# Kernel tuning notes

Hardware: AMD Instinct MI355X
Metric: run time of the kernel (lower is better)

Reference implementation:

```python
import jax, jax.numpy as jnp
import numpy as np

B, S, A, C, M, CE = 2, 8, 24000, 80, 20, 7
POS_TH, NEG_TH = 0.5, 0.4
V0, V1 = 0.1, 0.2              # SSD encode variances
SL1_BETA = 1.0 / 9.0
ALPHA, GAMMA = 0.25, 2.0
CB_BETA = 0.9999
EPS = 1e-7


def point_form(cf):
    # (cx,cy,w,h) -> (x1,y1,x2,y2)
    return jnp.concatenate([cf[..., :2] - cf[..., 2:] * 0.5, cf[..., :2] + cf[..., 2:] * 0.5], -1)


def jaccard(a, b):
    # a: [M,4], b: [A,4] point form -> IoU [M,A]
    lt = jnp.maximum(a[:, None, :2], b[None, :, :2])
    rb = jnp.minimum(a[:, None, 2:], b[None, :, 2:])
    wh = jnp.clip(rb - lt, 0.0)
    inter = wh[..., 0] * wh[..., 1]
    aa = (a[:, 2] - a[:, 0]) * (a[:, 3] - a[:, 1])
    ab = (b[:, 2] - b[:, 0]) * (b[:, 3] - b[:, 1])
    return inter / (aa[:, None] + ab[None, :] - inter + 1e-10)


def encode(matched, anchors_cf):
    # matched: [A,4] point form gt, anchors_cf: [A,4] center form
    g_cxcy = ((matched[:, :2] + matched[:, 2:]) * 0.5 - anchors_cf[:, :2]) / (V0 * anchors_cf[:, 2:])
    g_wh = jnp.log(jnp.clip(matched[:, 2:] - matched[:, :2], 1e-6) / anchors_cf[:, 2:]) / V1
    return jnp.concatenate([g_cxcy, g_wh], -1)


def bce(p, y):
    p = jnp.clip(p, EPS, 1.0 - EPS)
    return -(y * jnp.log(p) + (1.0 - y) * jnp.log1p(-p))


def match_one(gtb, gtl, count, anchors_pf, anchors_cf):
    # SSD-style match with ignore band: conf in {-1 ignore, 0 background, i+1 positive matched to gt i}
    valid = jnp.arange(M) < count
    iou = jnp.where(valid[:, None], jaccard(gtb, anchors_pf), -1.0)  # [M,A]
    best_prior_idx = jnp.argmax(iou, axis=1)                         # best anchor per gt
    best_truth_iou = jnp.max(iou, axis=0)                            # best gt per anchor
    best_truth_idx = jnp.argmax(iou, axis=0)
    sidx = jnp.where(valid, best_prior_idx, A)                       # out-of-range -> dropped
    best_truth_iou = best_truth_iou.at[sidx].set(2.0, mode='drop')   # force each gt's best anchor positive
    best_truth_idx = best_truth_idx.at[sidx].set(jnp.arange(M), mode='drop')
    conf = (best_truth_idx + 1).astype(jnp.int32)                    # dummy labels = gt index
    conf = jnp.where(best_truth_iou < POS_TH, -1, conf)
    conf = jnp.where(best_truth_iou < NEG_TH, 0, conf)
    loc = encode(gtb[best_truth_idx], anchors_cf)
    has = count > 0
    conf = jnp.where(has, conf, -1)                                  # empty frame -> all ignore
    loc = jnp.where(has, loc, 0.0)
    # gather per-anchor multi-hot labels: labels_bs = [zeros; gt_labels][dumy_conf]
    lab = jnp.where((conf > 0)[:, None], gtl[jnp.clip(conf - 1, 0, M - 1)], 0.0)
    return conf, loc, lab


def setup_inputs() -> dict:
    key = jax.random.key(0)
    ks = jax.random.split(key, 10)
    confidence = jax.random.normal(ks[0], (B, S, A, C), jnp.float32)
    predicted_locations = jax.random.normal(ks[1], (B, S, A, 4), jnp.float32)
    gc = jax.random.uniform(ks[2], (B, S, M, 2))
    gw = jax.random.uniform(ks[3], (B, S, M, 2), minval=0.05, maxval=0.4)
    gt_boxes = jnp.clip(jnp.concatenate([gc - gw * 0.5, gc + gw * 0.5], -1), 0.0, 1.0)
    gt_labels = (jax.random.uniform(ks[4], (B, S, M, C)) < 0.05).astype(jnp.float32)
    counts = jax.random.randint(ks[5], (B, S), 0, M + 1, jnp.int32)
    ac = jax.random.uniform(ks[6], (A, 2))
    aw = jax.random.uniform(ks[7], (A, 2), minval=0.02, maxval=0.3)
    anchors = jnp.concatenate([ac, aw], -1)  # center form (cx,cy,w,h)
    ego_preds = jax.random.normal(ks[8], (B, S, CE), jnp.float32)
    ego_labels = jax.random.randint(ks[9], (B, S), 0, CE, jnp.int32)
    cls_num_list = jax.random.randint(jax.random.fold_in(key, 11), (C,), 1, 10000, jnp.int32)
    return {"confidence": confidence, "predicted_locations": predicted_locations,
            "gt_boxes": gt_boxes, "gt_labels": gt_labels, "counts": counts,
            "anchors": anchors, "ego_preds": ego_preds, "ego_labels": ego_labels,
            "cls_num_list": cls_num_list}


def reference(confidence, predicted_locations, gt_boxes, gt_labels, counts, anchors, ego_preds, ego_labels, cls_num_list):
    preds = jax.nn.sigmoid(confidence)
    anchors_pf = point_form(anchors)
    flat = lambda x: x.reshape((B * S,) + x.shape[2:])
    conf_t, loc_t, lab_t = jax.vmap(match_one, in_axes=(0, 0, 0, None, None))(
        flat(gt_boxes), flat(gt_labels), counts.reshape(-1), anchors_pf, anchors)
    labels_bin = jax.lax.stop_gradient(conf_t.reshape(B, S, A).astype(jnp.float32))
    gt_locations = jax.lax.stop_gradient(loc_t.reshape(B, S, A, 4))
    all_labels = jax.lax.stop_gradient(lab_t.reshape(B, S, A, C))

    pos = (labels_bin > 0).astype(jnp.float32)
    num_pos = jnp.maximum(1.0, pos.sum())
    n = jnp.abs(predicted_locations - gt_locations)
    sl1 = jnp.where(n < SL1_BETA, 0.5 * n * n / SL1_BETA, n - 0.5 * SL1_BETA)
    regression_loss = (sl1 * pos[..., None]).sum() / (num_pos * 4.0)

    # class-balanced focal loss (module hardcodes gamma=1 inside sigmoid_cb_focal_loss)
    cmask = (labels_bin > -1).astype(jnp.float32)[..., None]
    w = (1.0 - CB_BETA) / (1.0 - jnp.power(jnp.float32(CB_BETA), cls_num_list.astype(jnp.float32)))
    w = w / w.sum()
    y = all_labels
    pt = preds * y + (1.0 - preds) * (1.0 - y)
    cb = w * y + (1.0 - CB_BETA) * (1.0 - y)
    cls_loss = (bce(preds, y) * cb * (1.0 - pt) * cmask).sum() / num_pos

    # ego focal loss (replicates original get_one_hot_labels column semantics)
    ep = jax.nn.sigmoid(ego_preds)
    evalid = ego_labels > -1
    col = (jnp.where(evalid[..., None], jax.nn.one_hot(ego_labels, CE), 0.0).sum((0, 1)) > 0).astype(jnp.float32)
    oh = jnp.broadcast_to(col, ep.shape)
    af = ALPHA * oh + (1.0 - ALPHA) * (1.0 - oh)
    ept = ep * oh + (1.0 - ep) * (1.0 - oh)
    n_ego = evalid.sum().astype(jnp.float32)
    ego_sum = (bce(ep, oh) * af * (1.0 - ept) ** GAMMA * evalid[..., None].astype(jnp.float32)).sum()
    ego_loss = jnp.where(n_ego > 0, ego_sum / jnp.maximum(n_ego, 1.0), 0.0)

    return regression_loss, cls_loss / 8.0 + ego_loss / 4.0
```

## Files before the change

kernel.cpp:

```cpp
#include <hip/hip_runtime.h>
#include <math.h>

#define NB 2
#define NS 8
#define NA 24000
#define NC 80
#define NM 20
#define NCE 7
#define NBS (NB*NS)
#define CPB 75
#define APC (NA/CPB)

#define POS_TH 0.5f
#define NEG_TH 0.4f
#define OMB 1e-4f
#define SL1B (1.0f/9.0f)

__device__ inline unsigned long long packKey(float f, unsigned idx) {
    unsigned u = __float_as_uint(f);
    u = (u & 0x80000000u) ? ~u : (u | 0x80000000u);
    return ((unsigned long long)u << 32) | (unsigned long long)(0xFFFFFFFFu - idx);
}

__global__ void __launch_bounds__(256)
k_mega(const float* __restrict__ gtb, const int* __restrict__ counts,
       const float* __restrict__ anchors, const float* __restrict__ ploc,
       const float* __restrict__ gtl, const float* __restrict__ logits,
       const int* __restrict__ cls_num, unsigned long long* __restrict__ gbest,
       double* __restrict__ acc, int* __restrict__ npos) {
    __shared__ float sg[NM][5];
    __shared__ unsigned long long sk[4][NM];
    __shared__ double sb[4];
    __shared__ float wsh[NC];
    __shared__ float wsum_sh;
    __shared__ unsigned qpos[APC];
    __shared__ unsigned qign[APC];
    __shared__ int npq, nqi;
    __shared__ float sf[4], sc[4];
    __shared__ int si[4];

    int bid = blockIdx.x;
    int role = bid % 3;
    int u = bid / 3;
    int bs = u / CPB, chunk = u % CPB;
    int t = threadIdx.x;
    int cnt = counts[bs];
    int a0 = chunk * APC;
    int wave = t >> 6, lane = t & 63;

    if (cnt == 0) return;

    if (role == 0) {
        const float4* x4p = (const float4*)logits + ((size_t)bs * NA + a0) * (NC / 4);
        double bg = 0.0;
        #pragma unroll
        for (int g = 0; g < 5; g++) {
            float4 xs[5];
            #pragma unroll
            for (int j = 0; j < 5; j++) xs[j] = x4p[t + (g * 5 + j) * 256];
            #pragma unroll
            for (int j = 0; j < 5; j++) {
                float xv[4] = {xs[j].x, xs[j].y, xs[j].z, xs[j].w};
                float tsum = 0.0f;
                #pragma unroll
                for (int jj = 0; jj < 4; jj++) {
                    float x = xv[jj];
                    float e = __expf(-x);
                    float s = 1.0f + e;
                    float pr = __builtin_amdgcn_rcpf(s);
                    float ls = __logf(s);
                    tsum += (x + ls) * pr;
                }
                bg += (double)tsum;
            }
        }
        #pragma unroll
        for (int off = 32; off > 0; off >>= 1) bg += __shfl_xor(bg, off);
        if (lane == 0) sb[wave] = bg;
        __syncthreads();
        if (t == 0) atomicAdd(&acc[1], (double)OMB * (sb[0] + sb[1] + sb[2] + sb[3]));
        return;
    }

    if (role == 2) {
        if (t < NM) {
            const float* g = gtb + ((size_t)bs * NM + t) * 4;
            float x1 = g[0], y1 = g[1], x2 = g[2], y2 = g[3];
            sg[t][0] = x1; sg[t][1] = y1; sg[t][2] = x2; sg[t][3] = y2;
            sg[t][4] = (x2 - x1) * (y2 - y1);
        }
        __syncthreads();
        bool has2 = t < (APC - 256);
        float4 c1 = ((const float4*)anchors)[a0 + t];
        float bx1 = c1.x - c1.z * 0.5f, by1 = c1.y - c1.w * 0.5f;
        float bx2 = c1.x + c1.z * 0.5f, by2 = c1.y + c1.w * 0.5f;
        float bar = (bx2 - bx1) * (by2 - by1);
        float cx1 = 0, cy1 = 0, cx2 = 0, cy2 = 0, car = 0;
        if (has2) {
            float4 c2 = ((const float4*)anchors)[a0 + 256 + t];
            cx1 = c2.x - c2.z * 0.5f; cy1 = c2.y - c2.w * 0.5f;
            cx2 = c2.x + c2.z * 0.5f; cy2 = c2.y + c2.w * 0.5f;
            car = (cx2 - cx1) * (cy2 - cy1);
        }
        for (int m = 0; m < cnt; m++) {
            float gx1 = sg[m][0], gy1 = sg[m][1], gx2 = sg[m][2], gy2 = sg[m][3], gar = sg[m][4];
            float ltx = fmaxf(gx1, bx1), lty = fmaxf(gy1, by1);
            float rbx = fminf(gx2, bx2), rby = fminf(gy2, by2);
            float wx = fmaxf(rbx - ltx, 0.0f), wy = fmaxf(rby - lty, 0.0f);
            float inter = wx * wy;
            float iou = inter / (gar + bar - inter + 1e-10f);
            unsigned long long k = packKey(iou, (unsigned)(a0 + t));
            if (has2) {
                float ltx2 = fmaxf(gx1, cx1), lty2 = fmaxf(gy1, cy1);
                float rbx2 = fminf(gx2, cx2), rby2 = fminf(gy2, cy2);
                float wx2 = fmaxf(rbx2 - ltx2, 0.0f), wy2 = fmaxf(rby2 - lty2, 0.0f);
                float inter2 = wx2 * wy2;
                float iou2 = inter2 / (gar + car - inter2 + 1e-10f);
                unsigned long long k2 = packKey(iou2, (unsigned)(a0 + 256 + t));
                if (k2 > k) k = k2;
            }
            #pragma unroll
            for (int off = 32; off > 0; off >>= 1) {
                unsigned long long o = __shfl_xor(k, off);
                if (o > k) k = o;
            }
            if (lane == 0) sk[wave][m] = k;
        }
        __syncthreads();
        if (t < cnt) {
            unsigned long long k = sk[0][t];
            if (sk[1][t] > k) k = sk[1][t];
            if (sk[2][t] > k) k = sk[2][t];
            if (sk[3][t] > k) k = sk[3][t];
            atomicMax(&gbest[bs * NM + t], k);
        }
        return;
    }

    if (t == 0) { npq = 0; nqi = 0; }
    if (t < NM) {
        const float* g = gtb + ((size_t)bs * NM + t) * 4;
        float x1 = g[0], y1 = g[1], x2 = g[2], y2 = g[3];
        sg[t][0] = x1; sg[t][1] = y1; sg[t][2] = x2; sg[t][3] = y2;
        sg[t][4] = (x2 - x1) * (y2 - y1);
    }
    if (t < NC) {
        float n = (float)cls_num[t];
        wsh[t] = OMB / (1.0f - powf(0.9999f, n));
    }
    __syncthreads();
    if (t == 0) {
        float s = 0.0f;
        for (int c = 0; c < NC; c++) s += wsh[c];
        wsum_sh = s;
    }
    __syncthreads();
    if (t < NC) wsh[t] = wsh[t] / wsum_sh;

    float regsum = 0.0f;
    int pcnt = 0;
    for (int al = t; al < APC; al += 256) {
        int a = a0 + al;
        float4 cf = ((const float4*)anchors)[a];
        float ax1 = cf.x - cf.z * 0.5f, ay1 = cf.y - cf.w * 0.5f;
        float ax2 = cf.x + cf.z * 0.5f, ay2 = cf.y + cf.w * 0.5f;
        float aarea = (ax2 - ax1) * (ay2 - ay1);
        float best = -1.0f; int bm = 0;
        for (int m = 0; m < cnt; m++) {
            float ltx = fmaxf(sg[m][0], ax1), lty = fmaxf(sg[m][1], ay1);
            float rbx = fminf(sg[m][2], ax2), rby = fminf(sg[m][3], ay2);
            float wx = fmaxf(rbx - ltx, 0.0f), wy = fmaxf(rby - lty, 0.0f);
            float inter = wx * wy;
            float iou = inter / (sg[m][4] + aarea - inter + 1e-10f);
            if (iou > best) { best = iou; bm = m; }
        }
        int code = (best < NEG_TH) ? 0 : (best < POS_TH) ? -1 : bm + 1;
        if (code > 0) {
            pcnt++;
            size_t ia = (size_t)bs * NA + a;
            float mx1 = sg[bm][0], my1 = sg[bm][1], mx2 = sg[bm][2], my2 = sg[bm][3];
            float g0 = ((mx1 + mx2) * 0.5f - cf.x) / (0.1f * cf.z);
            float g1 = ((my1 + my2) * 0.5f - cf.y) / (0.1f * cf.w);
            float g2 = logf(fmaxf(mx2 - mx1, 1e-6f) / cf.z) / 0.2f;
            float g3 = logf(fmaxf(my2 - my1, 1e-6f) / cf.w) / 0.2f;
            float4 p = ((const float4*)ploc)[ia];
            float n0 = fabsf(p.x - g0), n1 = fabsf(p.y - g1);
            float n2 = fabsf(p.z - g2), n3 = fabsf(p.w - g3);
            float s0 = n0 < SL1B ? 0.5f * n0 * n0 / SL1B : n0 - 0.5f * SL1B;
            float s1 = n1 < SL1B ? 0.5f * n1 * n1 / SL1B : n1 - 0.5f * SL1B;
            float s2 = n2 < SL1B ? 0.5f * n2 * n2 / SL1B : n2 - 0.5f * SL1B;
            float s3 = n3 < SL1B ? 0.5f * n3 * n3 / SL1B : n3 - 0.5f * SL1B;
            regsum += s0 + s1 + s2 + s3;
            int q = atomicAdd(&npq, 1);
            qpos[q] = ((unsigned)bm << 16) | (unsigned)al;
        } else if (code == -1) {
            int q = atomicAdd(&nqi, 1);
            qign[q] = (unsigned)al;
        }
    }
    __syncthreads();

    float corrsum = 0.0f;
    int nq = npq, ni = nqi;
    for (int i = t; i < nq * 20; i += 256) {
        int qq = i / 20, c4 = i % 20;
        unsigned e = qpos[qq];
        int al = e & 0xFFFFu;
        int m  = (int)(e >> 16);
        float4 y4 = ((const float4*)(gtl + ((size_t)(bs * NM + m)) * NC))[c4];
        if (y4.x > 0.5f || y4.y > 0.5f || y4.z > 0.5f || y4.w > 0.5f) {
            float4 x4 = ((const float4*)logits)[((size_t)bs * NA + a0 + al) * (NC / 4) + c4];
            float yv[4] = {y4.x, y4.y, y4.z, y4.w};
            float xv[4] = {x4.x, x4.y, x4.z, x4.w};
            #pragma unroll
            for (int j = 0; j < 4; j++) {
                if (yv[j] > 0.5f) {
                    float x = xv[j];
                    float ee = __expf(-x);
                    float s = 1.0f + ee;
                    float pr = __builtin_amdgcn_rcpf(s);
                    float ls = __logf(s);
                    corrsum += ls * wsh[c4 * 4 + j] * (ee * pr)
                             - OMB * (x + ls) * pr;
                }
            }
        }
    }
    float negsum = 0.0f;
    for (int i = t; i < ni * 20; i += 256) {
        int qq = i / 20, c4 = i % 20;
        int al = (int)qign[qq];
        float4 x4 = ((const float4*)logits)[((size_t)bs * NA + a0 + al) * (NC / 4) + c4];
        float xv[4] = {x4.x, x4.y, x4.z, x4.w};
        float rs = 0.0f;
        #pragma unroll
        for (int j = 0; j < 4; j++) {
            float x = xv[j];
            float e = __expf(-x);
            float s = 1.0f + e;
            float pr = __builtin_amdgcn_rcpf(s);
            float ls = __logf(s);
            rs += (x + ls) * pr;
        }
        negsum += rs;
    }
    float clssum = corrsum - OMB * negsum;

    #pragma unroll
    for (int off = 32; off > 0; off >>= 1) {
        regsum += __shfl_xor(regsum, off);
        clssum += __shfl_xor(clssum, off);
        pcnt   += __shfl_xor(pcnt, off);
    }
    if (lane == 0) { sf[wave] = regsum; sc[wave] = clssum; si[wave] = pcnt; }
    __syncthreads();
    if (t == 0) {
        atomicAdd(&acc[0], (double)(sf[0] + sf[1] + sf[2] + sf[3]));
        atomicAdd(&acc[1], (double)(sc[0] + sc[1] + sc[2] + sc[3]));
        atomicAdd(npos, si[0] + si[1] + si[2] + si[3]);
    }
}

__global__ void __launch_bounds__(256)
k_final(const float* __restrict__ gtb, const int* __restrict__ counts,
        const float* __restrict__ anchors, const float* __restrict__ ploc,
        const float* __restrict__ gtl, const float* __restrict__ logits,
        const int* __restrict__ cls_num, const unsigned long long* __restrict__ gbest,
        const float* __restrict__ ego_preds, const int* __restrict__ ego_labels,
        const double* __restrict__ acc, const int* __restrict__ npos,
        float* __restrict__ out) {
    __shared__ float sg[NBS][NM][5];
    __shared__ unsigned sA[NBS][NM];
    __shared__ int scnt[NBS];
    __shared__ float wsh[NC];
    __shared__ float wsum_sh;
    __shared__ float scol[NCE];
    __shared__ float sdr[256], sdc[256];
    __shared__ int sdn[256];
    __shared__ float sred[256];
    __shared__ int sval[256];
    const float EPSF = 1e-7f;
    int t = threadIdx.x;

    if (t < NBS) scnt[t] = counts[t];
    if (t < NC) {
        float n = (float)cls_num[t];
        wsh[t] = OMB / (1.0f - powf(0.9999f, n));
    }
    if (t < NCE) {
        float c = 0.0f;
        for (int i = 0; i < NBS; i++) {
            int l = ego_labels[i];
            if (l > -1 && l == t) c = 1.0f;
        }
        scol[t] = c;
    }
    __syncthreads();
    if (t < NBS * NM) {
        int bs = t / NM, m = t % NM;
        const float* g = gtb + (size_t)t * 4;
        float x1 = g[0], y1 = g[1], x2 = g[2], y2 = g[3];
        sg[bs][m][0] = x1; sg[bs][m][1] = y1; sg[bs][m][2] = x2; sg[bs][m][3] = y2;
        sg[bs][m][4] = (x2 - x1) * (y2 - y1);
        sA[bs][m] = (m < scnt[bs])
            ? (unsigned)(0xFFFFFFFFu - (unsigned)(gbest[t] & 0xFFFFFFFFull))
            : 0xFFFFFFFFu;
    }
    if (t == 0) {
        float s = 0.0f;
        for (int c = 0; c < NC; c++) s += wsh[c];
        wsum_sh = s;
    }
    __syncthreads();
    if (t < NC) wsh[t] = wsh[t] / wsum_sh;
    __syncthreads();

    float dreg = 0.0f, dcls = 0.0f; int dnp = 0;
    if (t < NBS * NM) {
        int bs = t / NM, m = t % NM;
        int cnt = scnt[bs];
        if (m < cnt) {
            unsigned a = sA[bs][m];
            bool overridden = false;
            for (int m2 = m + 1; m2 < cnt; m2++)
                if (sA[bs][m2] == a) overridden = true;
            if (!overridden) {
                float4 cf = ((const float4*)anchors)[a];
                float ax1 = cf.x - cf.z * 0.5f, ay1 = cf.y - cf.w * 0.5f;
                float ax2 = cf.x + cf.z * 0.5f, ay2 = cf.y + cf.w * 0.5f;
                float aarea = (ax2 - ax1) * (ay2 - ay1);
                float best = -1.0f; int bm = 0;
                for (int m2 = 0; m2 < cnt; m2++) {
                    float ltx = fmaxf(sg[bs][m2][0], ax1), lty = fmaxf(sg[bs][m2][1], ay1);
                    float rbx = fminf(sg[bs][m2][2], ax2), rby = fminf(sg[bs][m2][3], ay2);
                    float wx = fmaxf(rbx - ltx, 0.0f), wy = fmaxf(rby - lty, 0.0f);
                    float inter = wx * wy;
                    float iou = inter / (sg[bs][m2][4] + aarea - inter + 1e-10f);
                    if (iou > best) { best = iou; bm = m2; }
                }
                int code = (best < NEG_TH) ? 0 : (best < POS_TH) ? -1 : bm + 1;
                if (!(code > 0 && bm == m)) {
                    size_t ia = (size_t)bs * NA + a;
                    float4 p = ((const float4*)ploc)[ia];
                    auto sl1 = [&](int mm) -> float {
                        float mx1 = sg[bs][mm][0], my1 = sg[bs][mm][1];
                        float mx2 = sg[bs][mm][2], my2 = sg[bs][mm][3];
                        float g0 = ((mx1 + mx2) * 0.5f - cf.x) / (0.1f * cf.z);
                        float g1 = ((my1 + my2) * 0.5f - cf.y) / (0.1f * cf.w);
                        float g2 = logf(fmaxf(mx2 - mx1, 1e-6f) / cf.z) / 0.2f;
                        float g3 = logf(fmaxf(my2 - my1, 1e-6f) / cf.w) / 0.2f;
                        float n0 = fabsf(p.x - g0), n1 = fabsf(p.y - g1);
                        float n2 = fabsf(p.z - g2), n3 = fabsf(p.w - g3);
                        float s0 = n0 < SL1B ? 0.5f * n0 * n0 / SL1B : n0 - 0.5f * SL1B;
                        float s1 = n1 < SL1B ? 0.5f * n1 * n1 / SL1B : n1 - 0.5f * SL1B;
                        float s2 = n2 < SL1B ? 0.5f * n2 * n2 / SL1B : n2 - 0.5f * SL1B;
                        float s3 = n3 < SL1B ? 0.5f * n3 * n3 / SL1B : n3 - 0.5f * SL1B;
                        return s0 + s1 + s2 + s3;
                    };
                    dreg += sl1(m);
                    if (code > 0) dreg -= sl1(bm);
                    else dnp += 1;
                    const float* xrow = logits + ia * NC;
                    const float* ynew = gtl + ((size_t)(bs * NM + m)) * NC;
                    const float* yold = gtl + ((size_t)(bs * NM + bm)) * NC;
                    bool addbg = (code == -1);
                    for (int c = 0; c < NC; c++) {
                        float x = xrow[c];
                        float e = __expf(-x);
                        float s = 1.0f + e;
                        float pr = __builtin_amdgcn_rcpf(s);
                        float ls = __logf(s);
                        float bgterm = OMB * (x + ls) * pr;
                        if (addbg) dcls += bgterm;
                        if (ynew[c] > 0.5f)
                            dcls += ls * wsh[c] * (e * pr) - bgterm;
                        if (code > 0 && yold[c] > 0.5f)
                            dcls -= ls * wsh[c] * (e * pr) - bgterm;
                    }
                }
            }
        }
    }
    sdr[t] = dreg; sdc[t] = dcls; sdn[t] = dnp;

    float term = 0.0f;
    if (t < NBS * NCE) {
        int bs = t / NCE, e = t % NCE;
        int lbl = ego_labels[bs];
        if (lbl > -1) {
            float x = ego_preds[t];
            float ep = 1.0f / (1.0f + expf(-x));
            float oh = scol[e];
            float af = 0.25f * oh + 0.75f * (1.0f - oh);
            float ept = ep * oh + (1.0f - ep) * (1.0f - oh);
            float epc = fminf(fmaxf(ep, EPSF), 1.0f - EPSF);
            float bce = -(oh * logf(epc) + (1.0f - oh) * log1pf(-epc));
            float om = 1.0f - ept;
            term = bce * af * om * om;
        }
    }
    sred[t] = term;
    sval[t] = (t < NBS && ego_labels[t] > -1) ? 1 : 0;
    __syncthreads();
    for (int off = 128; off > 0; off >>= 1) {
        if (t < off) {
            sdr[t] += sdr[t + off]; sdc[t] += sdc[t + off]; sdn[t] += sdn[t + off];
            sred[t] += sred[t + off]; sval[t] += sval[t + off];
        }
        __syncthreads();
    }
    if (t == 0) {
        float esum = sred[0];
        int ne = sval[0];
        float ego = (ne > 0) ? esum / (float)(ne > 1 ? ne : 1) : 0.0f;
        double npd = (double)(*npos + sdn[0]);
        if (npd < 1.0) npd = 1.0;
        double regT = acc[0] + (double)sdr[0];
        double clsT = acc[1] + (double)sdc[0];
        out[0] = (float)(regT / (npd * 4.0));
        out[1] = (float)(clsT / npd / 8.0 + (double)ego / 4.0);
    }
}

extern "C" void kernel_launch(void* const* d_in, const int* in_sizes, int n_in,
                              void* d_out, int out_size, void* d_ws, size_t ws_size,
                              hipStream_t stream) {
    const float* confidence = (const float*)d_in[0];
    const float* ploc       = (const float*)d_in[1];
    const float* gtb        = (const float*)d_in[2];
    const float* gtl        = (const float*)d_in[3];
    const int*   counts     = (const int*)d_in[4];
    const float* anchors    = (const float*)d_in[5];
    const float* ego_preds  = (const float*)d_in[6];
    const int*   ego_labels = (const int*)d_in[7];
    const int*   cls_num    = (const int*)d_in[8];
    float* out = (float*)d_out;

    char* ws = (char*)d_ws;
    double* acc  = (double*)ws;
    int* npos    = (int*)(ws + 16);
    unsigned long long* gbest = (unsigned long long*)(ws + 64);

    hipMemsetAsync(ws, 0, 4096, stream);
    k_mega<<<3 * NBS * CPB, 256, 0, stream>>>(gtb, counts, anchors, ploc, gtl,
                                              confidence, cls_num, gbest, acc, npos);
    k_final<<<1, 256, 0, stream>>>(gtb, counts, anchors, ploc, gtl, confidence,
                                   cls_num, gbest, ego_preds, ego_labels,
                                   acc, npos, out);
}
```

Baseline: 261.5 us.

## Replace global atomics and memset with per-block partials reduced in final kernel

Each block now writes its per-chunk best-anchor keys and its regression, classification and positive-count partials to dedicated workspace slots, instead of doing atomicAdd/atomicMax into shared global accumulators. The final single-block kernel reduces these partials, which removes the hipMemsetAsync launch and the global atomic contention. The background-logit loop is also restructured into a double-buffered issue/consume pattern to overlap loads with the transcendental math. In exchange, the final kernel must now scan 75 chunk entries per gt and about 3600 partials serially in one block.

New measurement: 244.6 us. 6.5% less time.

```diff
diff --git a/kernel.cpp b/kernel.cpp
--- a/kernel.cpp
+++ b/kernel.cpp
@@ -10,6 +10,7 @@
 #define NBS (NB*NS)
 #define CPB 75
 #define APC (NA/CPB)
+#define NUNITS (3*NBS*CPB)
 
 #define POS_TH 0.5f
 #define NEG_TH 0.4f
@@ -26,8 +27,9 @@
 k_mega(const float* __restrict__ gtb, const int* __restrict__ counts,
        const float* __restrict__ anchors, const float* __restrict__ ploc,
        const float* __restrict__ gtl, const float* __restrict__ logits,
-       const int* __restrict__ cls_num, unsigned long long* __restrict__ gbest,
-       double* __restrict__ acc, int* __restrict__ npos) {
+       const int* __restrict__ cls_num,
+       unsigned long long* __restrict__ chunkbest,
+       double* __restrict__ regp, double* __restrict__ clsp, int* __restrict__ npp) {
     __shared__ float sg[NM][5];
     __shared__ unsigned long long sk[4][NM];
     __shared__ double sb[4];
@@ -41,248 +43,262 @@
 
     int bid = blockIdx.x;
     int role = bid % 3;
-    int u = bid / 3;
-    int bs = u / CPB, chunk = u % CPB;
+    int unit = bid / 3;
+    int bs = unit / CPB, chunk = unit % CPB;
     int t = threadIdx.x;
     int cnt = counts[bs];
     int a0 = chunk * APC;
     int wave = t >> 6, lane = t & 63;
 
-    if (cnt == 0) return;
-
-    if (role == 0) {
-        const float4* x4p = (const float4*)logits + ((size_t)bs * NA + a0) * (NC / 4);
-        double bg = 0.0;
-        #pragma unroll
-        for (int g = 0; g < 5; g++) {
-            float4 xs[5];
+    double accReg = 0.0, accCls = 0.0;
+    int accNp = 0;
+
+    if (cnt != 0) {
+        if (role == 0) {
+            const float4* x4p = (const float4*)logits + ((size_t)bs * NA + a0) * (NC / 4);
+            float4 xa[5], xb[5];
+            double bg = 0.0;
+#define ISSUE(ARR,B) { _Pragma("unroll") \
+            for (int j = 0; j < 5; j++) ARR[j] = x4p[t + ((B)*5 + j)*256]; }
+#define CONSUME(ARR) { _Pragma("unroll") \
+            for (int j = 0; j < 5; j++) { \
+                float xv[4] = {ARR[j].x, ARR[j].y, ARR[j].z, ARR[j].w}; \
+                float tsum = 0.0f; \
+                _Pragma("unroll") \
+                for (int jj = 0; jj < 4; jj++) { \
+                    float x = xv[jj]; \
+                    float e = __expf(-x); \
+                    float s = 1.0f + e; \
+                    float pr = __builtin_amdgcn_rcpf(s); \
+                    float ls = __logf(s); \
+                    tsum += (x + ls) * pr; \
+                } \
+                bg += (double)tsum; \
+            } }
+            ISSUE(xa, 0);
+            ISSUE(xb, 1); CONSUME(xa);
+            ISSUE(xa, 2); CONSUME(xb);
+            ISSUE(xb, 3); CONSUME(xa);
+            ISSUE(xa, 4); CONSUME(xb);
+            CONSUME(xa);
+#undef ISSUE
+#undef CONSUME
             #pragma unroll
-            for (int j = 0; j < 5; j++) xs[j] = x4p[t + (g * 5 + j) * 256];
-            #pragma unroll
-            for (int j = 0; j < 5; j++) {
-                float xv[4] = {xs[j].x, xs[j].y, xs[j].z, xs[j].w};
-                float tsum = 0.0f;
+            for (int off = 32; off > 0; off >>= 1) bg += __shfl_xor(bg, off);
+            if (lane == 0) sb[wave] = bg;
+            __syncthreads();
+            if (t == 0) accCls = (double)OMB * (sb[0] + sb[1] + sb[2] + sb[3]);
+        } else if (role == 2) {
+            if (t < NM) {
+                const float* g = gtb + ((size_t)bs * NM + t) * 4;
+                float x1 = g[0], y1 = g[1], x2 = g[2], y2 = g[3];
+                sg[t][0] = x1; sg[t][1] = y1; sg[t][2] = x2; sg[t][3] = y2;
+                sg[t][4] = (x2 - x1) * (y2 - y1);
+            }
+            __syncthreads();
+            bool has2 = t < (APC - 256);
+            float4 c1 = ((const float4*)anchors)[a0 + t];
+            float bx1 = c1.x - c1.z * 0.5f, by1 = c1.y - c1.w * 0.5f;
+            float bx2 = c1.x + c1.z * 0.5f, by2 = c1.y + c1.w * 0.5f;
+            float bar = (bx2 - bx1) * (by2 - by1);
+            float cx1 = 0, cy1 = 0, cx2 = 0, cy2 = 0, car = 0;
+            if (has2) {
+                float4 c2 = ((const float4*)anchors)[a0 + 256 + t];
+                cx1 = c2.x - c2.z * 0.5f; cy1 = c2.y - c2.w * 0.5f;
+                cx2 = c2.x + c2.z * 0.5f; cy2 = c2.y + c2.w * 0.5f;
+                car = (cx2 - cx1) * (cy2 - cy1);
+            }
+            for (int m = 0; m < cnt; m++) {
+                float gx1 = sg[m][0], gy1 = sg[m][1], gx2 = sg[m][2], gy2 = sg[m][3], gar = sg[m][4];
+                float ltx = fmaxf(gx1, bx1), lty = fmaxf(gy1, by1);
+                float rbx = fminf(gx2, bx2), rby = fminf(gy2, by2);
+                float wx = fmaxf(rbx - ltx, 0.0f), wy = fmaxf(rby - lty, 0.0f);
+                float inter = wx * wy;
+                float iou = inter / (gar + bar - inter + 1e-10f);
+                unsigned long long k = packKey(iou, (unsigned)(a0 + t));
+                if (has2) {
+                    float ltx2 = fmaxf(gx1, cx1), lty2 = fmaxf(gy1, cy1);
+                    float rbx2 = fminf(gx2, cx2), rby2 = fminf(gy2, cy2);
+                    float wx2 = fmaxf(rbx2 - ltx2, 0.0f), wy2 = fmaxf(rby2 - lty2, 0.0f);
+                    float inter2 = wx2 * wy2;
+                    float iou2 = inter2 / (gar + car - inter2 + 1e-10f);
+                    unsigned long long k2 = packKey(iou2, (unsigned)(a0 + 256 + t));
+                    if (k2 > k) k = k2;
+                }
                 #pragma unroll
-                for (int jj = 0; jj < 4; jj++) {
-                    float x = xv[jj];
+                for (int off = 32; off > 0; off >>= 1) {
+                    unsigned long long o = __shfl_xor(k, off);
+                    if (o > k) k = o;
+                }
+                if (lane == 0) sk[wave][m] = k;
+            }
+            __syncthreads();
+            if (t < NM) {
+                unsigned long long k = 0ULL;
+                if (t < cnt) {
+                    k = sk[0][t];
+                    if (sk[1][t] > k) k = sk[1][t];
+                    if (sk[2][t] > k) k = sk[2][t];
+                    if (sk[3][t] > k) k = sk[3][t];
+                }
+                chunkbest[(size_t)unit * NM + t] = k;
+            }
+        } else {
+            if (t == 0) { npq = 0; nqi = 0; }
+            if (t < NM) {
+                const float* g = gtb + ((size_t)bs * NM + t) * 4;
+                float x1 = g[0], y1 = g[1], x2 = g[2], y2 = g[3];
+                sg[t][0] = x1; sg[t][1] = y1; sg[t][2] = x2; sg[t][3] = y2;
+                sg[t][4] = (x2 - x1) * (y2 - y1);
+            }
+            if (t < NC) {
+                float n = (float)cls_num[t];
+                wsh[t] = OMB / (1.0f - powf(0.9999f, n));
+            }
+            __syncthreads();
+            if (t == 0) {
+                float s = 0.0f;
+                for (int c = 0; c < NC; c++) s += wsh[c];
+                wsum_sh = s;
+            }
+            __syncthreads();
+            if (t < NC) wsh[t] = wsh[t] / wsum_sh;
+
+            float regsum = 0.0f;
+            int pcnt = 0;
+            for (int al = t; al < APC; al += 256) {
+                int a = a0 + al;
+                float4 cf = ((const float4*)anchors)[a];
+                float ax1 = cf.x - cf.z * 0.5f, ay1 = cf.y - cf.w * 0.5f;
+                float ax2 = cf.x + cf.z * 0.5f, ay2 = cf.y + cf.w * 0.5f;
+                float aarea = (ax2 - ax1) * (ay2 - ay1);
+                float best = -1.0f; int bm = 0;
+                for (int m = 0; m < cnt; m++) {
+                    float ltx = fmaxf(sg[m][0], ax1), lty = fmaxf(sg[m][1], ay1);
+                    float rbx = fminf(sg[m][2], ax2), rby = fminf(sg[m][3], ay2);
+                    float wx = fmaxf(rbx - ltx, 0.0f), wy = fmaxf(rby - lty, 0.0f);
+                    float inter = wx * wy;
+                    float iou = inter / (sg[m][4] + aarea - inter + 1e-10f);
+                    if (iou > best) { best = iou; bm = m; }
+                }
+                int code = (best < NEG_TH) ? 0 : (best < POS_TH) ? -1 : bm + 1;
+                if (code > 0) {
+                    pcnt++;
+                    size_t ia = (size_t)bs * NA + a;
+                    float mx1 = sg[bm][0], my1 = sg[bm][1], mx2 = sg[bm][2], my2 = sg[bm][3];
+                    float g0 = ((mx1 + mx2) * 0.5f - cf.x) / (0.1f * cf.z);
+                    float g1 = ((my1 + my2) * 0.5f - cf.y) / (0.1f * cf.w);
+                    float g2 = logf(fmaxf(mx2 - mx1, 1e-6f) / cf.z) / 0.2f;
+                    float g3 = logf(fmaxf(my2 - my1, 1e-6f) / cf.w) / 0.2f;
+                    float4 p = ((const float4*)ploc)[ia];
+                    float n0 = fabsf(p.x - g0), n1 = fabsf(p.y - g1);
+                    float n2 = fabsf(p.z - g2), n3 = fabsf(p.w - g3);
+                    float s0 = n0 < SL1B ? 0.5f * n0 * n0 / SL1B : n0 - 0.5f * SL1B;
+                    float s1 = n1 < SL1B ? 0.5f * n1 * n1 / SL1B : n1 - 0.5f * SL1B;
+                    float s2 = n2 < SL1B ? 0.5f * n2 * n2 / SL1B : n2 - 0.5f * SL1B;
+                    float s3 = n3 < SL1B ? 0.5f * n3 * n3 / SL1B : n3 - 0.5f * SL1B;
+                    regsum += s0 + s1 + s2 + s3;
+                    int q = atomicAdd(&npq, 1);
+                    qpos[q] = ((unsigned)bm << 16) | (unsigned)al;
+                } else if (code == -1) {
+                    int q = atomicAdd(&nqi, 1);
+                    qign[q] = (unsigned)al;
+                }
+            }
+            __syncthreads();
+
+            float corrsum = 0.0f;
+            int nq = npq, ni = nqi;
+            for (int i = t; i < nq * 20; i += 256) {
+                int qq = i / 20, c4 = i % 20;
+                unsigned e = qpos[qq];
+                int al = e & 0xFFFFu;
+                int m  = (int)(e >> 16);
+                float4 y4 = ((const float4*)(gtl + ((size_t)(bs * NM + m)) * NC))[c4];
+                if (y4.x > 0.5f || y4.y > 0.5f || y4.z > 0.5f || y4.w > 0.5f) {
+                    float4 x4 = ((const float4*)logits)[((size_t)bs * NA + a0 + al) * (NC / 4) + c4];
+                    float yv[4] = {y4.x, y4.y, y4.z, y4.w};
+                    float xv[4] = {x4.x, x4.y, x4.z, x4.w};
+                    #pragma unroll
+                    for (int j = 0; j < 4; j++) {
+                        if (yv[j] > 0.5f) {
+                            float x = xv[j];
+                            float ee = __expf(-x);
+                            float s = 1.0f + ee;
+                            float pr = __builtin_amdgcn_rcpf(s);
+                            float ls = __logf(s);
+                            corrsum += ls * wsh[c4 * 4 + j] * (ee * pr)
+                                     - OMB * (x + ls) * pr;
+                        }
+                    }
+                }
+            }
+            float negsum = 0.0f;
+            for (int i = t; i < ni * 20; i += 256) {
+                int qq = i / 20, c4 = i % 20;
+                int al = (int)qign[qq];
+                float4 x4 = ((const float4*)logits)[((size_t)bs * NA + a0 + al) * (NC / 4) + c4];
+                float xv[4] = {x4.x, x4.y, x4.z, x4.w};
+                float rs = 0.0f;
+                #pragma unroll
+                for (int j = 0; j < 4; j++) {
+                    float x = xv[j];
                     float e = __expf(-x);
                     float s = 1.0f + e;
                     float pr = __builtin_amdgcn_rcpf(s);
                     float ls = __logf(s);
-                    tsum += (x + ls) * pr;
-                }
-                bg += (double)tsum;
-            }
-        }
-        #pragma unroll
-        for (int off = 32; off > 0; off >>= 1) bg += __shfl_xor(bg, off);
-        if (lane == 0) sb[wave] = bg;
-        __syncthreads();
-        if (t == 0) atomicAdd(&acc[1], (double)OMB * (sb[0] + sb[1] + sb[2] + sb[3]));
-        return;
-    }
-
-    if (role == 2) {
-        if (t < NM) {
-            const float* g = gtb + ((size_t)bs * NM + t) * 4;
-            float x1 = g[0], y1 = g[1], x2 = g[2], y2 = g[3];
-            sg[t][0] = x1; sg[t][1] = y1; sg[t][2] = x2; sg[t][3] = y2;
-            sg[t][4] = (x2 - x1) * (y2 - y1);
-        }
-        __syncthreads();
-        bool has2 = t < (APC - 256);
-        float4 c1 = ((const float4*)anchors)[a0 + t];
-        float bx1 = c1.x - c1.z * 0.5f, by1 = c1.y - c1.w * 0.5f;
-        float bx2 = c1.x + c1.z * 0.5f, by2 = c1.y + c1.w * 0.5f;
-        float bar = (bx2 - bx1) * (by2 - by1);
-        float cx1 = 0, cy1 = 0, cx2 = 0, cy2 = 0, car = 0;
-        if (has2) {
-            float4 c2 = ((const float4*)anchors)[a0 + 256 + t];
-            cx1 = c2.x - c2.z * 0.5f; cy1 = c2.y - c2.w * 0.5f;
-            cx2 = c2.x + c2.z * 0.5f; cy2 = c2.y + c2.w * 0.5f;
-            car = (cx2 - cx1) * (cy2 - cy1);
-        }
-        for (int m = 0; m < cnt; m++) {
-            float gx1 = sg[m][0], gy1 = sg[m][1], gx2 = sg[m][2], gy2 = sg[m][3], gar = sg[m][4];
-            float ltx = fmaxf(gx1, bx1), lty = fmaxf(gy1, by1);
-            float rbx = fminf(gx2, bx2), rby = fminf(gy2, by2);
-            float wx = fmaxf(rbx - ltx, 0.0f), wy = fmaxf(rby - lty, 0.0f);
-            float inter = wx * wy;
-            float iou = inter / (gar + bar - inter + 1e-10f);
-            unsigned long long k = packKey(iou, (unsigned)(a0 + t));
-            if (has2) {
-                float ltx2 = fmaxf(gx1, cx1), lty2 = fmaxf(gy1, cy1);
-                float rbx2 = fminf(gx2, cx2), rby2 = fminf(gy2, cy2);
-                float wx2 = fmaxf(rbx2 - ltx2, 0.0f), wy2 = fmaxf(rby2 - lty2, 0.0f);
-                float inter2 = wx2 * wy2;
-                float iou2 = inter2 / (gar + car - inter2 + 1e-10f);
-                unsigned long long k2 = packKey(iou2, (unsigned)(a0 + 256 + t));
-                if (k2 > k) k = k2;
-            }
+                    rs += (x + ls) * pr;
+                }
+                negsum += rs;
+            }
+            float clssum = corrsum - OMB * negsum;
+
             #pragma unroll
             for (int off = 32; off > 0; off >>= 1) {
-                unsigned long long o = __shfl_xor(k, off);
-                if (o > k) k = o;
-            }
-            if (lane == 0) sk[wave][m] = k;
-        }
-        __syncthreads();
-        if (t < cnt) {
-            unsigned long long k = sk[0][t];
-            if (sk[1][t] > k) k = sk[1][t];
-            if (sk[2][t] > k) k = sk[2][t];
-            if (sk[3][t] > k) k = sk[3][t];
-            atomicMax(&gbest[bs * NM + t], k);
-        }
-        return;
-    }
-
-    if (t == 0) { npq = 0; nqi = 0; }
-    if (t < NM) {
-        const float* g = gtb + ((size_t)bs * NM + t) * 4;
-        float x1 = g[0], y1 = g[1], x2 = g[2], y2 = g[3];
-        sg[t][0] = x1; sg[t][1] = y1; sg[t][2] = x2; sg[t][3] = y2;
-        sg[t][4] = (x2 - x1) * (y2 - y1);
-    }
-    if (t < NC) {
-        float n = (float)cls_num[t];
-        wsh[t] = OMB / (1.0f - powf(0.9999f, n));
-    }
-    __syncthreads();
-    if (t == 0) {
-        float s = 0.0f;
-        for (int c = 0; c < NC; c++) s += wsh[c];
-        wsum_sh = s;
-    }
-    __syncthreads();
-    if (t < NC) wsh[t] = wsh[t] / wsum_sh;
-
-    float regsum = 0.0f;
-    int pcnt = 0;
-    for (int al = t; al < APC; al += 256) {
-        int a = a0 + al;
-        float4 cf = ((const float4*)anchors)[a];
-        float ax1 = cf.x - cf.z * 0.5f, ay1 = cf.y - cf.w * 0.5f;
-        float ax2 = cf.x + cf.z * 0.5f, ay2 = cf.y + cf.w * 0.5f;
-        float aarea = (ax2 - ax1) * (ay2 - ay1);
-        float best = -1.0f; int bm = 0;
-        for (int m = 0; m < cnt; m++) {
-            float ltx = fmaxf(sg[m][0], ax1), lty = fmaxf(sg[m][1], ay1);
-            float rbx = fminf(sg[m][2], ax2), rby = fminf(sg[m][3], ay2);
-            float wx = fmaxf(rbx - ltx, 0.0f), wy = fmaxf(rby - lty, 0.0f);
-            float inter = wx * wy;
-            float iou = inter / (sg[m][4] + aarea - inter + 1e-10f);
-            if (iou > best) { best = iou; bm = m; }
-        }
-        int code = (best < NEG_TH) ? 0 : (best < POS_TH) ? -1 : bm + 1;
-        if (code > 0) {
-            pcnt++;
-            size_t ia = (size_t)bs * NA + a;
-            float mx1 = sg[bm][0], my1 = sg[bm][1], mx2 = sg[bm][2], my2 = sg[bm][3];
-            float g0 = ((mx1 + mx2) * 0.5f - cf.x) / (0.1f * cf.z);
-            float g1 = ((my1 + my2) * 0.5f - cf.y) / (0.1f * cf.w);
-            float g2 = logf(fmaxf(mx2 - mx1, 1e-6f) / cf.z) / 0.2f;
-            float g3 = logf(fmaxf(my2 - my1, 1e-6f) / cf.w) / 0.2f;
-            float4 p = ((const float4*)ploc)[ia];
-            float n0 = fabsf(p.x - g0), n1 = fabsf(p.y - g1);
-            float n2 = fabsf(p.z - g2), n3 = fabsf(p.w - g3);
-            float s0 = n0 < SL1B ? 0.5f * n0 * n0 / SL1B : n0 - 0.5f * SL1B;
-            float s1 = n1 < SL1B ? 0.5f * n1 * n1 / SL1B : n1 - 0.5f * SL1B;
-            float s2 = n2 < SL1B ? 0.5f * n2 * n2 / SL1B : n2 - 0.5f * SL1B;
-            float s3 = n3 < SL1B ? 0.5f * n3 * n3 / SL1B : n3 - 0.5f * SL1B;
-            regsum += s0 + s1 + s2 + s3;
-            int q = atomicAdd(&npq, 1);
-            qpos[q] = ((unsigned)bm << 16) | (unsigned)al;
-        } else if (code == -1) {
-            int q = atomicAdd(&nqi, 1);
-            qign[q] = (unsigned)al;
-        }
-    }
-    __syncthreads();
-
-    float corrsum = 0.0f;
-    int nq = npq, ni = nqi;
-    for (int i = t; i < nq * 20; i += 256) {
-        int qq = i / 20, c4 = i % 20;
-        unsigned e = qpos[qq];
-        int al = e & 0xFFFFu;
-        int m  = (int)(e >> 16);
-        float4 y4 = ((const float4*)(gtl + ((size_t)(bs * NM + m)) * NC))[c4];
-        if (y4.x > 0.5f || y4.y > 0.5f || y4.z > 0.5f || y4.w > 0.5f) {
-            float4 x4 = ((const float4*)logits)[((size_t)bs * NA + a0 + al) * (NC / 4) + c4];
-            float yv[4] = {y4.x, y4.y, y4.z, y4.w};
-            float xv[4] = {x4.x, x4.y, x4.z, x4.w};
-            #pragma unroll
-            for (int j = 0; j < 4; j++) {
-                if (yv[j] > 0.5f) {
-                    float x = xv[j];
-                    float ee = __expf(-x);
-                    float s = 1.0f + ee;
-                    float pr = __builtin_amdgcn_rcpf(s);
-                    float ls = __logf(s);
-                    corrsum += ls * wsh[c4 * 4 + j] * (ee * pr)
-                             - OMB * (x + ls) * pr;
-                }
-            }
-        }
-    }
-    float negsum = 0.0f;
-    for (int i = t; i < ni * 20; i += 256) {
-        int qq = i / 20, c4 = i % 20;
-        int al = (int)qign[qq];
-        float4 x4 = ((const float4*)logits)[((size_t)bs * NA + a0 + al) * (NC / 4) + c4];
-        float xv[4] = {x4.x, x4.y, x4.z, x4.w};
-        float rs = 0.0f;
-        #pragma unroll
-        for (int j = 0; j < 4; j++) {
-            float x = xv[j];
-            float e = __expf(-x);
-            float s = 1.0f + e;
-            float pr = __builtin_amdgcn_rcpf(s);
-            float ls = __logf(s);
-            rs += (x + ls) * pr;
-        }
-        negsum += rs;
-    }
-    float clssum = corrsum - OMB * negsum;
-
-    #pragma unroll
-    for (int off = 32; off > 0; off >>= 1) {
-        regsum += __shfl_xor(regsum, off);
-        clssum += __shfl_xor(clssum, off);
-        pcnt   += __shfl_xor(pcnt, off);
-    }
-    if (lane == 0) { sf[wave] = regsum; sc[wave] = clssum; si[wave] = pcnt; }
-    __syncthreads();
-    if (t == 0) {
-        atomicAdd(&acc[0], (double)(sf[0] + sf[1] + sf[2] + sf[3]));
-        atomicAdd(&acc[1], (double)(sc[0] + sc[1] + sc[2] + sc[3]));
-        atomicAdd(npos, si[0] + si[1] + si[2] + si[3]);
-    }
+                regsum += __shfl_xor(regsum, off);
+                clssum += __shfl_xor(clssum, off);
+                pcnt   += __shfl_xor(pcnt, off);
+            }
+            if (lane == 0) { sf[wave] = regsum; sc[wave] = clssum; si[wave] = pcnt; }
+            __syncthreads();
+            if (t == 0) {
+                accReg = (double)(sf[0] + sf[1] + sf[2] + sf[3]);
+                accCls = (double)(sc[0] + sc[1] + sc[2] + sc[3]);
+                accNp  = si[0] + si[1] + si[2] + si[3];
+            }
+        }
+    }
+
+    if (t == 0) { regp[bid] = accReg; clsp[bid] = accCls; npp[bid] = accNp; }
 }
 
 __global__ void __launch_bounds__(256)
 k_final(const float* __restrict__ gtb, const int* __restrict__ counts,
         const float* __restrict__ anchors, const float* __restrict__ ploc,
         const float* __restrict__ gtl, const float* __restrict__ logits,
-        const int* __restrict__ cls_num, const unsigned long long* __restrict__ gbest,
+        const int* __restrict__ cls_num,
+        const unsigned long long* __restrict__ chunkbest,
+        const double* __restrict__ regp, const double* __restrict__ clsp,
+        const int* __restrict__ npp,
         const float* __restrict__ ego_preds, const int* __restrict__ ego_labels,
-        const double* __restrict__ acc, const int* __restrict__ npos,
         float* __restrict__ out) {
-    __shared__ float sg[NBS][NM][5];
-    __shared__ unsigned sA[NBS][NM];
-    __shared__ int scnt[NBS];
+    __shared__ float sg2[NBS][NM][5];
+    __shared__ unsigned sA2[NBS][NM];
+    __shared__ int scnt2[NBS];
     __shared__ float wsh[NC];
     __shared__ float wsum_sh;
-    __shared__ float scol[NCE];
+    __shared__ float scol2[NCE];
     __shared__ float sdr[256], sdc[256];
     __shared__ int sdn[256];
-    __shared__ float sred[256];
-    __shared__ int sval[256];
+    __shared__ float sred2[256];
+    __shared__ int sval2[256];
+    __shared__ double spr[4], spc[4];
+    __shared__ int spn[4];
     const float EPSF = 1e-7f;
     int t = threadIdx.x;
-
-    if (t < NBS) scnt[t] = counts[t];
+    int wave = t >> 6, lane = t & 63;
+
+    if (t < NBS) scnt2[t] = counts[t];
     if (t < NC) {
         float n = (float)cls_num[t];
         wsh[t] = OMB / (1.0f - powf(0.9999f, n));
@@ -293,18 +309,25 @@
             int l = ego_labels[i];
             if (l > -1 && l == t) c = 1.0f;
         }
-        scol[t] = c;
+        scol2[t] = c;
     }
     __syncthreads();
-    if (t < NBS * NM) {
-        int bs = t / NM, m = t % NM;
-        const float* g = gtb + (size_t)t * 4;
+    for (int p = t; p < NBS * NM; p += 256) {
+        int bs = p / NM, m = p % NM;
+        const float* g = gtb + (size_t)p * 4;
         float x1 = g[0], y1 = g[1], x2 = g[2], y2 = g[3];
-        sg[bs][m][0] = x1; sg[bs][m][1] = y1; sg[bs][m][2] = x2; sg[bs][m][3] = y2;
-        sg[bs][m][4] = (x2 - x1) * (y2 - y1);
-        sA[bs][m] = (m < scnt[bs])
-            ? (unsigned)(0xFFFFFFFFu - (unsigned)(gbest[t] & 0xFFFFFFFFull))
-            : 0xFFFFFFFFu;
+        sg2[bs][m][0] = x1; sg2[bs][m][1] = y1; sg2[bs][m][2] = x2; sg2[bs][m][3] = y2;
+        sg2[bs][m][4] = (x2 - x1) * (y2 - y1);
+        unsigned amin = 0xFFFFFFFFu;
+        if (m < scnt2[bs]) {
+            unsigned long long k = 0ULL;
+            for (int c = 0; c < CPB; c++) {
+                unsigned long long o = chunkbest[((size_t)(bs * CPB + c)) * NM + m];
+                if (o > k) k = o;
+            }
+            amin = 0xFFFFFFFFu - (unsigned)(k & 0xFFFFFFFFull);
+        }
+        sA2[bs][m] = amin;
     }
     if (t == 0) {
         float s = 0.0f;
@@ -315,15 +338,25 @@
     if (t < NC) wsh[t] = wsh[t] / wsum_sh;
     __syncthreads();
 
+    double pr_ = 0.0, pc_ = 0.0; int pn_ = 0;
+    for (int i = t; i < NUNITS; i += 256) { pr_ += regp[i]; pc_ += clsp[i]; pn_ += npp[i]; }
+    #pragma unroll
+    for (int off = 32; off > 0; off >>= 1) {
+        pr_ += __shfl_xor(pr_, off);
+        pc_ += __shfl_xor(pc_, off);
+        pn_ += __shfl_xor(pn_, off);
+    }
+    if (lane == 0) { spr[wave] = pr_; spc[wave] = pc_; spn[wave] = pn_; }
+
     float dreg = 0.0f, dcls = 0.0f; int dnp = 0;
-    if (t < NBS * NM) {
-        int bs = t / NM, m = t % NM;
-        int cnt = scnt[bs];
+    for (int p = t; p < NBS * NM; p += 256) {
+        int bs = p / NM, m = p % NM;
+        int cnt = scnt2[bs];
         if (m < cnt) {
-            unsigned a = sA[bs][m];
+            unsigned a = sA2[bs][m];
             bool overridden = false;
             for (int m2 = m + 1; m2 < cnt; m2++)
-                if (sA[bs][m2] == a) overridden = true;
+                if (sA2[bs][m2] == a) overridden = true;
             if (!overridden) {
                 float4 cf = ((const float4*)anchors)[a];
                 float ax1 = cf.x - cf.z * 0.5f, ay1 = cf.y - cf.w * 0.5f;
@@ -331,26 +364,26 @@
                 float aarea = (ax2 - ax1) * (ay2 - ay1);
                 float best = -1.0f; int bm = 0;
                 for (int m2 = 0; m2 < cnt; m2++) {
-                    float ltx = fmaxf(sg[bs][m2][0], ax1), lty = fmaxf(sg[bs][m2][1], ay1);
-                    float rbx = fminf(sg[bs][m2][2], ax2), rby = fminf(sg[bs][m2][3], ay2);
+                    float ltx = fmaxf(sg2[bs][m2][0], ax1), lty = fmaxf(sg2[bs][m2][1], ay1);
+                    float rbx = fminf(sg2[bs][m2][2], ax2), rby = fminf(sg2[bs][m2][3], ay2);
                     float wx = fmaxf(rbx - ltx, 0.0f), wy = fmaxf(rby - lty, 0.0f);
                     float inter = wx * wy;
-                    float iou = inter / (sg[bs][m2][4] + aarea - inter + 1e-10f);
+                    float iou = inter / (sg2[bs][m2][4] + aarea - inter + 1e-10f);
                     if (iou > best) { best = iou; bm = m2; }
                 }
                 int code = (best < NEG_TH) ? 0 : (best < POS_TH) ? -1 : bm + 1;
                 if (!(code > 0 && bm == m)) {
                     size_t ia = (size_t)bs * NA + a;
-                    float4 p = ((const float4*)ploc)[ia];
+                    float4 pv = ((const float4*)ploc)[ia];
                     auto sl1 = [&](int mm) -> float {
-                        float mx1 = sg[bs][mm][0], my1 = sg[bs][mm][1];
-                        float mx2 = sg[bs][mm][2], my2 = sg[bs][mm][3];
+                        float mx1 = sg2[bs][mm][0], my1 = sg2[bs][mm][1];
+                        float mx2 = sg2[bs][mm][2], my2 = sg2[bs][mm][3];
                         float g0 = ((mx1 + mx2) * 0.5f - cf.x) / (0.1f * cf.z);
                         float g1 = ((my1 + my2) * 0.5f - cf.y) / (0.1f * cf.w);
                         float g2 = logf(fmaxf(mx2 - mx1, 1e-6f) / cf.z) / 0.2f;
                         float g3 = logf(fmaxf(my2 - my1, 1e-6f) / cf.w) / 0.2f;
-                        float n0 = fabsf(p.x - g0), n1 = fabsf(p.y - g1);
-                        float n2 = fabsf(p.z - g2), n3 = fabsf(p.w - g3);
+                        float n0 = fabsf(pv.x - g0), n1 = fabsf(pv.y - g1);
+                        float n2 = fabsf(pv.z - g2), n3 = fabsf(pv.w - g3);
                         float s0 = n0 < SL1B ? 0.5f * n0 * n0 / SL1B : n0 - 0.5f * SL1B;
                         float s1 = n1 < SL1B ? 0.5f * n1 * n1 / SL1B : n1 - 0.5f * SL1B;
                         float s2 = n2 < SL1B ? 0.5f * n2 * n2 / SL1B : n2 - 0.5f * SL1B;
@@ -390,7 +423,7 @@
         if (lbl > -1) {
             float x = ego_preds[t];
             float ep = 1.0f / (1.0f + expf(-x));
-            float oh = scol[e];
+            float oh = scol2[e];
             float af = 0.25f * oh + 0.75f * (1.0f - oh);
             float ept = ep * oh + (1.0f - ep) * (1.0f - oh);
             float epc = fminf(fmaxf(ep, EPSF), 1.0f - EPSF);
@@ -399,24 +432,24 @@
             term = bce * af * om * om;
         }
     }
-    sred[t] = term;
-    sval[t] = (t < NBS && ego_labels[t] > -1) ? 1 : 0;
+    sred2[t] = term;
+    sval2[t] = (t < NBS && ego_labels[t] > -1) ? 1 : 0;
     __syncthreads();
     for (int off = 128; off > 0; off >>= 1) {
         if (t < off) {
             sdr[t] += sdr[t + off]; sdc[t] += sdc[t + off]; sdn[t] += sdn[t + off];
-            sred[t] += sred[t + off]; sval[t] += sval[t + off];
+            sred2[t] += sred2[t + off]; sval2[t] += sval2[t + off];
         }
         __syncthreads();
     }
     if (t == 0) {
-        float esum = sred[0];
-        int ne = sval[0];
+        float esum = sred2[0];
+        int ne = sval2[0];
         float ego = (ne > 0) ? esum / (float)(ne > 1 ? ne : 1) : 0.0f;
-        double npd = (double)(*npos + sdn[0]);
+        double regT = (spr[0] + spr[1] + spr[2] + spr[3]) + (double)sdr[0];
+        double clsT = (spc[0] + spc[1] + spc[2] + spc[3]) + (double)sdc[0];
+        double npd = (double)((spn[0] + spn[1] + spn[2] + spn[3]) + sdn[0]);
         if (npd < 1.0) npd = 1.0;
-        double regT = acc[0] + (double)sdr[0];
-        double clsT = acc[1] + (double)sdc[0];
         out[0] = (float)(regT / (npd * 4.0));
         out[1] = (float)(clsT / npd / 8.0 + (double)ego / 4.0);
     }
@@ -437,14 +470,14 @@
     float* out = (float*)d_out;
 
     char* ws = (char*)d_ws;
-    double* acc  = (double*)ws;
-    int* npos    = (int*)(ws + 16);
-    unsigned long long* gbest = (unsigned long long*)(ws + 64);
-
-    hipMemsetAsync(ws, 0, 4096, stream);
-    k_mega<<<3 * NBS * CPB, 256, 0, stream>>>(gtb, counts, anchors, ploc, gtl,
-                                              confidence, cls_num, gbest, acc, npos);
+    unsigned long long* chunkbest = (unsigned long long*)ws;
+    double* regp = (double*)(ws + 192000);
+    double* clsp = (double*)(ws + 220800);
+    int*    npp  = (int*)(ws + 249600);
+
+    k_mega<<<NUNITS, 256, 0, stream>>>(gtb, counts, anchors, ploc, gtl, confidence,
+                                       cls_num, chunkbest, regp, clsp, npp);
     k_final<<<1, 256, 0, stream>>>(gtb, counts, anchors, ploc, gtl, confidence,
-                                   cls_num, gbest, ego_preds, ego_labels,
-                                   acc, npos, out);
+                                   cls_num, chunkbest, regp, clsp, npp,
+                                   ego_preds, ego_labels, out);
 }
```
